# Performance work log

Hardware: AMD Instinct MI355X
Metric: run time of the kernel (lower is better)

## Reference

```python
import jax, jax.numpy as jnp
import numpy as np
from jax import lax

B, S, I = 256, 16, 64
D = 128
N_ITEMS = 100000
K = 3
PAD_ID = 0
BOS_ID = N_ITEMS
DILATIONS = (1, 2, 4)


def setup_inputs() -> dict:
    key = jax.random.key(0)
    ks = jax.random.split(key, 16)
    item_id = jax.random.randint(ks[0], (B, S, I), 0, N_ITEMS, dtype=jnp.int32)
    eval_from = jax.random.randint(ks[1], (B,), 0, S, dtype=jnp.int32)
    u_type = jax.random.randint(ks[2], (B,), 0, 4, dtype=jnp.int32)
    emb = jax.random.normal(ks[3], (N_ITEMS + 1, D), jnp.float32) * 0.05
    emb = emb.at[PAD_ID].set(0.0)  # padding_idx=0
    kaiming = (2.0 / (D * K)) ** 0.5
    conv_w0 = jax.random.normal(ks[4], (D, D, K), jnp.float32) * kaiming
    conv_w1 = jax.random.normal(ks[5], (D, D, K), jnp.float32) * kaiming
    conv_w2 = jax.random.normal(ks[6], (D, D, K), jnp.float32) * kaiming
    conv_b0 = jnp.zeros((D,), jnp.float32)
    conv_b1 = jnp.zeros((D,), jnp.float32)
    conv_b2 = jnp.zeros((D,), jnp.float32)
    gru_wih = jax.random.normal(ks[7], (3 * D, D), jnp.float32) * 0.05
    gru_whh = jax.random.normal(ks[8], (3 * D, D), jnp.float32) * 0.05
    gru_bih = jax.random.normal(ks[9], (3 * D,), jnp.float32) * 0.05
    gru_bhh = jax.random.normal(ks[10], (3 * D,), jnp.float32) * 0.05
    fus_w = jax.random.normal(ks[11], (D, 2 * D), jnp.float32) * 0.05
    fus_b = jnp.zeros((D,), jnp.float32)
    return {"item_id": item_id, "eval_from": eval_from, "u_type": u_type,
            "emb": emb,
            "conv_w0": conv_w0, "conv_b0": conv_b0,
            "conv_w1": conv_w1, "conv_b1": conv_b1,
            "conv_w2": conv_w2, "conv_b2": conv_b2,
            "gru_wih": gru_wih, "gru_whh": gru_whh,
            "gru_bih": gru_bih, "gru_bhh": gru_bhh,
            "fus_w": fus_w, "fus_b": fus_b}


def reference(item_id, eval_from, u_type, emb,
              conv_w0, conv_b0, conv_w1, conv_b1, conv_w2, conv_b2,
              gru_wih, gru_whh, gru_bih, gru_bhh, fus_w, fus_b):
    item_id = jnp.maximum(item_id, 0)  # clamp_min(0)
    Bc, Sc, Ic = item_id.shape
    convs = ((conv_w0, conv_b0, DILATIONS[0]),
             (conv_w1, conv_b1, DILATIONS[1]),
             (conv_w2, conv_b2, DILATIONS[2]))

    def tcn(x):  # x: [B, T, D] -> [B, T, D]
        h = jnp.transpose(x, (0, 2, 1))  # NCH
        for w, b, dil in convs:
            pad = (K - 1) * dil
            out = lax.conv_general_dilated(
                h, w, window_strides=(1,), padding=[(pad, 0)],
                rhs_dilation=(dil,),
                dimension_numbers=('NCH', 'OIH', 'NCH')) + b[None, :, None]
            h = jax.nn.relu(out + h)
        return jnp.transpose(h, (0, 2, 1))

    def gru_step(h, x):  # h,x: [B, D]
        gi = x @ gru_wih.T + gru_bih
        gh = h @ gru_whh.T + gru_bhh
        ir, iz, inn = jnp.split(gi, 3, axis=-1)
        hr, hz, hn = jnp.split(gh, 3, axis=-1)
        r = jax.nn.sigmoid(ir + hr)
        z = jax.nn.sigmoid(iz + hz)
        n = jnp.tanh(inn + r * hn)
        return (1.0 - z) * n + z * h

    pos = jnp.arange(Ic + 1)
    bos = jnp.full((Bc, 1), BOS_ID, dtype=item_id.dtype)

    def step(h, seq_s):  # seq_s: [B, I]
        lengths = (seq_s != PAD_ID).sum(-1)          # [B]
        max_len = lengths.max()                       # batch-level session max
        seq = jnp.concatenate([bos, seq_s], axis=1)   # [B, I+1], BOS prepended
        valid = pos[None, :] <= max_len               # positions torch keeps
        seq = jnp.where(valid, seq, PAD_ID)
        mask = seq != PAD_ID
        e = emb[seq]                                  # [B, I+1, D] (PAD row is 0)
        tc = tcn(e)
        fin = jnp.concatenate([tc, jnp.broadcast_to(h[:, None, :], tc.shape)], -1)
        reps = fin @ fus_w.T + fus_b                  # [B, I+1, D]
        reps = reps * valid[..., None]                # torch zero-pads beyond max_len
        # drop mask at last valid token (per-sample python loop in torch)
        mask = mask & ~((pos[None, :] == lengths[:, None]) & (lengths > 0)[:, None])
        mf = mask.astype(e.dtype)
        mean_emb = (e * mf[..., None]).sum(1) / jnp.maximum(mf.sum(1), 1.0)[:, None]
        h2 = gru_step(h, mean_emb)
        return h2, (reps, mask)

    h0 = jnp.zeros((Bc, D), jnp.float32)
    _, (reps, masks) = lax.scan(step, h0, jnp.transpose(item_id, (1, 0, 2)))
    reps = jnp.transpose(reps, (1, 0, 2, 3))          # [B, S, I+1, D]
    masks = jnp.transpose(masks, (1, 0, 2))           # [B, S, I+1]
    allow = jnp.arange(Sc)[None, :] >= eval_from[:, None]
    loss_masks = masks & allow[:, :, None]
    return reps, loss_masks, u_type
```

## Files before the change

kernel.cpp:

```cpp
#include <hip/hip_runtime.h>

#define BB 256
#define SS 16
#define II 64
#define DD 128
#define TT 65
#define BOS_ID 100000
#define XROW 256
#define XROWS 73
#define XT (XROWS*XROW)

#define OFF_LEN  0
#define OFF_ML   16384
#define OFF_ME   32768
#define OFF_HB   (32768 + 2097152)
#define OFF_WB2  (OFF_HB + 2097152)
#define OFF_WIHP (OFF_WB2 + 327680)
#define OFF_WGRU (OFF_WIHP + 98304)
#define OFF_GI   (OFF_WGRU + 131072)

#define OUT_MASK  (BB*SS*TT*DD)
#define OUT_UTYPE (OUT_MASK + BB*SS*TT)

typedef __attribute__((ext_vector_type(8))) short short8;
typedef __attribute__((ext_vector_type(4))) float f32x4;

__device__ __forceinline__ unsigned short f2bf(float f) {
    unsigned int u = __builtin_bit_cast(unsigned int, f);
    return (unsigned short)((u + 0x7fffu + ((u >> 16) & 1u)) >> 16);
}
__device__ __forceinline__ float bflo(unsigned int u) {
    return __builtin_bit_cast(float, u << 16);
}
__device__ __forceinline__ float bfhi(unsigned int u) {
    return __builtin_bit_cast(float, u & 0xffff0000u);
}
__device__ __forceinline__ void gld16(const void* g, void* l) {
    __builtin_amdgcn_global_load_lds(
        (const __attribute__((address_space(1))) void*)g,
        (__attribute__((address_space(3))) void*)l, 16, 0, 0);
}

__global__ __launch_bounds__(256) void prep_kernel(
    const float* __restrict__ w0, const float* __restrict__ w1,
    const float* __restrict__ w2, const float* __restrict__ fus_w,
    const float* __restrict__ wih, const float* __restrict__ whh,
    unsigned short* __restrict__ wB2,
    unsigned int* __restrict__ wih4, unsigned int* __restrict__ wgru4)
{
    int idx = blockIdx.x * 256 + threadIdx.x;
    if (idx < 163840) {
        int cid2  = idx >> 11;
        int inner = idx & 2047;
        int g = inner >> 9;
        int c = (inner >> 3) & 63;
        int e = inner & 7;
        int nh   = cid2 & 1;
        int rest = cid2 >> 1;
        int cq   = rest & 3;
        int m    = rest >> 2;
        int ci = cq * 32 + g * 8 + e;
        int co = nh * 64 + c;
        float v;
        if (m < 9) {
            int L = m / 3, k = m % 3;
            const float* w = (L == 0) ? w0 : ((L == 1) ? w1 : w2);
            v = w[(co * 128 + ci) * 3 + k];
            if (k == 2 && ci == co) v += 1.0f;
        } else {
            v = fus_w[co * 256 + ci];
        }
        wB2[idx] = f2bf(v);
    } else if (idx < 163840 + 24576) {
        int f   = idx - 163840;
        int dd4 = f / 1536;
        int rem = f - dd4 * 1536;
        int r   = rem >> 2;
        int c   = rem & 3;
        int d0  = 8 * dd4 + 2 * c;
        unsigned int lo = f2bf(wih[r * 128 + d0]);
        unsigned int hi = f2bf(wih[r * 128 + d0 + 1]);
        wih4[f] = (hi << 16) | lo;
    } else if (idx < 163840 + 24576 + 32768) {
        int f   = idx - 163840 - 24576;
        int dd4 = f >> 11;
        int rem = f & 2047;
        int r   = rem >> 2;
        int c   = rem & 3;
        int d0  = 8 * dd4 + 2 * c;
        float v0, v1;
        if (r < 384) { v0 = whh[r * 128 + d0]; v1 = whh[r * 128 + d0 + 1]; }
        else { const float* fw = fus_w + (r - 384) * 256 + 128;
               v0 = fw[d0]; v1 = fw[d0 + 1]; }
        wgru4[f] = ((unsigned int)f2bf(v1) << 16) | (unsigned int)f2bf(v0);
    }
}

__global__ __launch_bounds__(256) void len_kernel(
    const int* __restrict__ item_id, const int* __restrict__ u_type,
    int* __restrict__ lengths, int* __restrict__ maxlen,
    float* __restrict__ u_out)
{
    int s = blockIdx.x;
    int b = threadIdx.x;
    const int* row = item_id + (b * SS + s) * II;
    int cnt = 0;
    for (int i = 0; i < II; ++i) cnt += (row[i] > 0);
    lengths[b * SS + s] = cnt;
    __shared__ int red[256];
    red[b] = cnt;
    __syncthreads();
    for (int off = 128; off > 0; off >>= 1) {
        if (b < off) red[b] = max(red[b], red[b + off]);
        __syncthreads();
    }
    if (b == 0) maxlen[s] = red[0];
    if (s == 0) u_out[b] = (float)u_type[b];
}

__global__ __launch_bounds__(128) void mean_kernel(
    const int* __restrict__ item_id, const int* __restrict__ eval_from,
    const float* __restrict__ emb,
    const int* __restrict__ lengths, const int* __restrict__ maxlen,
    float* __restrict__ mean_emb, float* __restrict__ mask_out)
{
    int bid = blockIdx.x;
    int b = bid >> 4, s = bid & 15;
    int tid = threadIdx.x;
    __shared__ int seqs[TT];
    __shared__ int msk[TT];
    int ml  = maxlen[s];
    int len = lengths[bid];
    int ef  = eval_from[b];
    if (tid < TT) {
        int v;
        if (tid == 0) v = BOS_ID;
        else { int it = item_id[bid * II + tid - 1]; v = it > 0 ? it : 0; }
        if (tid > ml) v = 0;
        int m = (v != 0) && !(tid == len && len > 0);
        seqs[tid] = v;
        msk[tid]  = m;
        mask_out[bid * TT + tid] = (m && (s >= ef)) ? 1.0f : 0.0f;
    }
    __syncthreads();
    int cnt = 0;
    for (int p = 0; p < TT; ++p) cnt += msk[p];
    float acc = 0.0f;
    int d = tid;
    for (int p = 0; p < TT; ++p) {
        if (msk[p]) acc += emb[seqs[p] * DD + d];
    }
    mean_emb[bid * DD + d] = acc / (float)max(cnt, 1);
}

__global__ __launch_bounds__(384, 1) void gi_kernel(
    const float* __restrict__ me_all, const unsigned int* __restrict__ wih4,
    const float* __restrict__ bih, float* __restrict__ gi_all)
{
    __shared__ __align__(16) unsigned int wl[16 * 384 * 4];
    __shared__ __align__(16) float me[DD];
    int t   = threadIdx.x;
    int blk = blockIdx.x;
    {
        const unsigned char* g = (const unsigned char*)wih4 + t * 16;
        unsigned char* l = (unsigned char*)wl + t * 16;
#pragma unroll
        for (int i = 0; i < 16; ++i) gld16(g + i * 6144, l + i * 6144);
    }
    float bi = bih[t];
    asm volatile("s_waitcnt vmcnt(0)" ::: "memory");
    __syncthreads();
    const uint4* wl4 = (const uint4*)wl;
    for (int q = 0; q < 16; ++q) {
        int bs = blk * 16 + q;
        if (t < DD) me[t] = me_all[bs * DD + t];
        __syncthreads();
        float acc = bi;
#pragma unroll
        for (int dd4 = 0; dd4 < 16; ++dd4) {
            uint4 u = wl4[dd4 * 384 + t];
            float4 h0 = *(const float4*)&me[8 * dd4];
            float4 h1 = *(const float4*)&me[8 * dd4 + 4];
            acc += bflo(u.x) * h0.x + bfhi(u.x) * h0.y;
            acc += bflo(u.y) * h0.z + bfhi(u.y) * h0.w;
            acc += bflo(u.z) * h1.x + bfhi(u.z) * h1.y;
            acc += bflo(u.w) * h1.z + bfhi(u.w) * h1.w;
        }
        gi_all[bs * 384 + t] = acc;
        __syncthreads();
    }
}

__global__ __launch_bounds__(512, 1) void gru_kernel(
    const unsigned int* __restrict__ wgru4, const float* __restrict__ bhh,
    const float* __restrict__ fus_b, const float* __restrict__ gi_all,
    float* __restrict__ hB)
{
    __shared__ __align__(16) unsigned int hpk[64];
    __shared__ float g_z[DD], g_inn[DD], g_hn[DD];
    int t = threadIdx.x;
    int b = blockIdx.x;
    int j = t & 127;
    int grp = t >> 7;

    uint4 w[16];
    const uint4* wg4 = (const uint4*)wgru4;
#pragma unroll
    for (int dd4 = 0; dd4 < 16; ++dd4) w[dd4] = wg4[dd4 * 512 + t];

    float gi_r[SS];
#pragma unroll
    for (int s = 0; s < SS; ++s)
        gi_r[s] = (grp < 3) ? gi_all[(b * SS + s) * 384 + t] : 0.0f;

    float bias = (t < 384) ? bhh[t] : fus_b[j];
    float hj = 0.0f;
    if (t < 64) hpk[t] = 0u;
    __syncthreads();

    for (int s = 0; s < SS; ++s) {
        float acc = bias;
#pragma unroll
        for (int dd4 = 0; dd4 < 16; ++dd4) {
            uint4 hp = *(const uint4*)&hpk[dd4 * 4];
            uint4 u  = w[dd4];
            acc += bflo(u.x) * bflo(hp.x) + bfhi(u.x) * bfhi(hp.x);
            acc += bflo(u.y) * bflo(hp.y) + bfhi(u.y) * bfhi(hp.y);
            acc += bflo(u.z) * bflo(hp.z) + bfhi(u.z) * bfhi(hp.z);
            acc += bflo(u.w) * bflo(hp.w) + bfhi(u.w) * bfhi(hp.w);
        }
        if (grp == 3) {
            hB[(s * BB + b) * DD + j] = acc;
        } else if (grp == 1) { g_z[j] = gi_r[s] + acc; }
        else if (grp == 2)   { g_inn[j] = gi_r[s]; g_hn[j] = acc; }
        __syncthreads();
        if (grp == 0) {
            float r = 1.0f / (1.0f + expf(-(gi_r[s] + acc)));
            float z = 1.0f / (1.0f + expf(-g_z[j]));
            float n = tanhf(g_inn[j] + r * g_hn[j]);
            float hnew = (1.0f - z) * n + z * hj;
            hj = hnew;
            float hnb = __shfl_xor(hnew, 1);
            if ((j & 1) == 0) {
                unsigned int pk;
                asm("v_cvt_pk_bf16_f32 %0, %1, %2" : "=v"(pk) : "v"(hnew), "v"(hnb));
                hpk[j >> 1] = pk;
            }
        }
        __syncthreads();
    }
}

__global__ __launch_bounds__(256, 3) void tcn_kernel(
    const int* __restrict__ item_id, const float* __restrict__ emb,
    const int* __restrict__ maxlen,
    const unsigned short* __restrict__ wB2,
    const float* __restrict__ cb0, const float* __restrict__ cb1,
    const float* __restrict__ cb2,
    const float* __restrict__ hB, float* __restrict__ reps)
{
    __shared__ __align__(16) unsigned char lds_x[2][XT];
    __shared__ __align__(16) unsigned char ring[2][8192];

    const int tid = threadIdx.x, bid = blockIdx.x;
    const int lane = tid & 63, wv = tid >> 6;
    const int l15 = lane & 15, q4 = lane >> 4;
    const int t = wv >> 1, nh = wv & 1;
    const int tile = bid * 2 + t;
    const int b = tile >> 4, s = tile & 15;
    const int ml = maxlen[s];

    const unsigned char* wgbase = (const unsigned char*)wB2;
    unsigned char* xb = lds_x[t];

    {
        const unsigned char* src = wgbase + wv * 1024 + lane * 16;
        gld16(src,        &ring[0][wv * 1024]);
        gld16(src + 4096, &ring[0][4096 + wv * 1024]);
    }
    int* seqs2 = (int*)&ring[1][0];
    if (tid < 2 * TT) {
        int tt = tid / TT, p = tid - tt * TT;
        int tl = bid * 2 + tt;
        int v;
        if (p == 0) v = BOS_ID;
        else { int it = item_id[tl * II + p - 1]; v = it > 0 ? it : 0; }
        if (p > maxlen[tl & 15]) v = 0;
        seqs2[tt * TT + p] = v;
    }
    {
        float4 z = {0.f, 0.f, 0.f, 0.f};
        if (tid < 128) *(float4*)(lds_x[0] + tid * 16) = z;
        else           *(float4*)(lds_x[1] + (tid - 128) * 16) = z;
    }
    __syncthreads();

    for (int p = nh; p < TT; p += 2) {
        const float* er = emb + (long)seqs2[t * TT + p] * DD + lane * 2;
        float f0 = er[0], f1 = er[1];
        unsigned int pk = ((unsigned int)f2bf(f1) << 16) | (unsigned int)f2bf(f0);
        *(unsigned int*)(xb + (8 + p) * XROW + ((lane * 4) ^ ((p & 7) << 4))) = pk;
    }

    f32x4 acc[5][4];

#pragma unroll 1
    for (int cid = 0; cid < 40; ++cid) {
        int L = 0, cq, off, kq = 0;
        if (cid < 36) { L = cid / 12; kq = cid - L * 12; int k = kq >> 2; cq = kq & 3; off = (2 - k) << L; }
        else { cq = cid - 36; off = 0; }
        if (cid == 36 || (cid < 36 && kq == 0)) {
#pragma unroll
            for (int mt = 0; mt < 5; ++mt)
#pragma unroll
                for (int nt = 0; nt < 4; ++nt)
#pragma unroll
                    for (int r = 0; r < 4; ++r) acc[mt][nt][r] = 0.0f;
        }
        asm volatile("s_waitcnt vmcnt(0)" ::: "memory");
        __syncthreads();

        if (cid <= 38) {
            const unsigned char* src =
                wgbase + (size_t)(cid + 1) * 8192 + wv * 1024 + lane * 16;
            gld16(src,        &ring[(cid + 1) & 1][wv * 1024]);
            gld16(src + 4096, &ring[(cid + 1) & 1][4096 + wv * 1024]);
        }

        const unsigned char* sb = &ring[cid & 1][nh * 4096];
        const int xmask = ((l15 - off) & 7) << 4;
        const int colx  = (cq * 64 + q4 * 16) ^ xmask;
        short8 bfr[4], af[5];
#pragma unroll
        for (int nt = 0; nt < 4; ++nt)
            bfr[nt] = *(const short8*)(sb + q4 * 1024 + (nt * 16 + l15) * 16);
#pragma unroll
        for (int mt = 0; mt < 5; ++mt) {
            int rowA = 8 + mt * 16 + l15 - off;
            af[mt] = *(const short8*)(xb + rowA * XROW + colx);
        }
#pragma unroll
        for (int nt = 0; nt < 4; ++nt)
#pragma unroll
            for (int mt = 0; mt < 5; ++mt)
                acc[mt][nt] = __builtin_amdgcn_mfma_f32_16x16x32_bf16(
                    af[mt], bfr[nt], acc[mt][nt], 0, 0, 0);

        if (cid < 36 && kq == 11) {
            const float* cb = (L == 0) ? cb0 : ((L == 1) ? cb1 : cb2);
            __syncthreads();
#pragma unroll
            for (int nt = 0; nt < 4; ++nt) {
                float bia = cb[nh * 64 + nt * 16 + l15];
                int cbyte = nh * 128 + nt * 32 + l15 * 2;
#pragma unroll
                for (int mt = 0; mt < 5; ++mt)
#pragma unroll
                    for (int r = 0; r < 4; ++r) {
                        int p = mt * 16 + q4 * 4 + r;
                        if (p < TT) {
                            int row = 8 + p;
                            float v = acc[mt][nt][r] + bia;
                            *(unsigned short*)(xb + row * XROW +
                                               (cbyte ^ ((row & 7) << 4))) =
                                f2bf(v > 0.f ? v : 0.f);
                        }
                    }
            }
            __syncthreads();
        }
    }

    float hb[4];
#pragma unroll
    for (int nt = 0; nt < 4; ++nt)
        hb[nt] = hB[(s * BB + b) * DD + nh * 64 + nt * 16 + l15];
    long ob = (long)tile * (TT * DD);
#pragma unroll
    for (int mt = 0; mt < 5; ++mt)
#pragma unroll
        for (int nt = 0; nt < 4; ++nt)
#pragma unroll
            for (int r = 0; r < 4; ++r) {
                int p = mt * 16 + q4 * 4 + r;
                if (p < TT) {
                    float v = (p <= ml) ? (acc[mt][nt][r] + hb[nt]) : 0.0f;
                    reps[ob + p * DD + nh * 64 + nt * 16 + l15] = v;
                }
            }
}

extern "C" void kernel_launch(void* const* d_in, const int* in_sizes, int n_in,
                              void* d_out, int out_size, void* d_ws, size_t ws_size,
                              hipStream_t stream) {
    const int*   item_id   = (const int*)  d_in[0];
    const int*   eval_from = (const int*)  d_in[1];
    const int*   u_type    = (const int*)  d_in[2];
    const float* emb       = (const float*)d_in[3];
    const float* conv_w0   = (const float*)d_in[4];
    const float* conv_b0   = (const float*)d_in[5];
    const float* conv_w1   = (const float*)d_in[6];
    const float* conv_b1   = (const float*)d_in[7];
    const float* conv_w2   = (const float*)d_in[8];
    const float* conv_b2   = (const float*)d_in[9];
    const float* gru_wih   = (const float*)d_in[10];
    const float* gru_whh   = (const float*)d_in[11];
    const float* gru_bih   = (const float*)d_in[12];
    const float* gru_bhh   = (const float*)d_in[13];
    const float* fus_w     = (const float*)d_in[14];
    const float* fus_b     = (const float*)d_in[15];

    char* ws = (char*)d_ws;
    int*            lengths  = (int*)           (ws + OFF_LEN);
    int*            maxlen   = (int*)           (ws + OFF_ML);
    float*          mean_emb = (float*)         (ws + OFF_ME);
    float*          hB       = (float*)         (ws + OFF_HB);
    unsigned short* wB2      = (unsigned short*)(ws + OFF_WB2);
    unsigned int*   wih4     = (unsigned int*)  (ws + OFF_WIHP);
    unsigned int*   wgru4    = (unsigned int*)  (ws + OFF_WGRU);
    float*          gi_all   = (float*)         (ws + OFF_GI);

    float* out  = (float*)d_out;
    float* reps = out;
    float* mout = out + OUT_MASK;
    float* uout = out + OUT_UTYPE;

    prep_kernel<<<864, 256, 0, stream>>>(conv_w0, conv_w1, conv_w2, fus_w,
                                         gru_wih, gru_whh, wB2, wih4, wgru4);
    len_kernel<<<SS, 256, 0, stream>>>(item_id, u_type, lengths, maxlen, uout);
    mean_kernel<<<BB * SS, 128, 0, stream>>>(item_id, eval_from, emb, lengths, maxlen,
                                             mean_emb, mout);
    gi_kernel<<<BB, 384, 0, stream>>>(mean_emb, wih4, gru_bih, gi_all);
    gru_kernel<<<BB, 512, 0, stream>>>(wgru4, gru_bhh, fus_b, gi_all, hB);
    tcn_kernel<<<BB * SS / 2, 256, 0, stream>>>(item_id, emb, maxlen, wB2,
                                                conv_b0, conv_b1, conv_b2, hB, reps);
}
```

Measured before the change: 253.8 us.

## Load TCN weight fragments directly into registers with one-step prefetch

Drops the LDS double-buffered weight ring, which used global-to-LDS loads plus a waitcnt and a block-wide barrier every chunk. Each lane now reads its B-operand MFMA fragments straight from global memory into registers and prefetches the next chunk's fragments while the current one is computed. This removes the per-chunk barrier and frees 16 KB of LDS, but each wave fetches its own weight copy from global or L2 and the extra live registers may hurt occupancy.

```diff
diff --git a/kernel.cpp b/kernel.cpp
--- a/kernel.cpp
+++ b/kernel.cpp
@@ -260,7 +260,7 @@
     const float* __restrict__ hB, float* __restrict__ reps)
 {
     __shared__ __align__(16) unsigned char lds_x[2][XT];
-    __shared__ __align__(16) unsigned char ring[2][8192];
+    __shared__ int seqs2[2][TT];
 
     const int tid = threadIdx.x, bid = blockIdx.x;
     const int lane = tid & 63, wv = tid >> 6;
@@ -270,15 +270,10 @@
     const int b = tile >> 4, s = tile & 15;
     const int ml = maxlen[s];
 
-    const unsigned char* wgbase = (const unsigned char*)wB2;
     unsigned char* xb = lds_x[t];
-
-    {
-        const unsigned char* src = wgbase + wv * 1024 + lane * 16;
-        gld16(src,        &ring[0][wv * 1024]);
-        gld16(src + 4096, &ring[0][4096 + wv * 1024]);
-    }
-    int* seqs2 = (int*)&ring[1][0];
+    const unsigned char* wfrag =
+        (const unsigned char*)wB2 + nh * 4096 + q4 * 1024 + l15 * 16;
+
     if (tid < 2 * TT) {
         int tt = tid / TT, p = tid - tt * TT;
         int tl = bid * 2 + tt;
@@ -286,21 +281,26 @@
         if (p == 0) v = BOS_ID;
         else { int it = item_id[tl * II + p - 1]; v = it > 0 ? it : 0; }
         if (p > maxlen[tl & 15]) v = 0;
-        seqs2[tt * TT + p] = v;
+        seqs2[tt][p] = v;
     }
     {
         float4 z = {0.f, 0.f, 0.f, 0.f};
         if (tid < 128) *(float4*)(lds_x[0] + tid * 16) = z;
         else           *(float4*)(lds_x[1] + (tid - 128) * 16) = z;
     }
+    short8 wcur[4];
+#pragma unroll
+    for (int nt = 0; nt < 4; ++nt)
+        wcur[nt] = *(const short8*)(wfrag + nt * 256);
     __syncthreads();
 
     for (int p = nh; p < TT; p += 2) {
-        const float* er = emb + (long)seqs2[t * TT + p] * DD + lane * 2;
+        const float* er = emb + (long)seqs2[t][p] * DD + lane * 2;
         float f0 = er[0], f1 = er[1];
         unsigned int pk = ((unsigned int)f2bf(f1) << 16) | (unsigned int)f2bf(f0);
         *(unsigned int*)(xb + (8 + p) * XROW + ((lane * 4) ^ ((p & 7) << 4))) = pk;
     }
+    __syncthreads();
 
     f32x4 acc[5][4];
 
@@ -317,23 +317,18 @@
 #pragma unroll
                     for (int r = 0; r < 4; ++r) acc[mt][nt][r] = 0.0f;
         }
-        asm volatile("s_waitcnt vmcnt(0)" ::: "memory");
-        __syncthreads();
-
-        if (cid <= 38) {
-            const unsigned char* src =
-                wgbase + (size_t)(cid + 1) * 8192 + wv * 1024 + lane * 16;
-            gld16(src,        &ring[(cid + 1) & 1][wv * 1024]);
-            gld16(src + 4096, &ring[(cid + 1) & 1][4096 + wv * 1024]);
-        }
-
-        const unsigned char* sb = &ring[cid & 1][nh * 4096];
+
+        short8 wnxt[4];
+        if (cid < 39) {
+            const unsigned char* src = wfrag + (size_t)(cid + 1) * 8192;
+#pragma unroll
+            for (int nt = 0; nt < 4; ++nt)
+                wnxt[nt] = *(const short8*)(src + nt * 256);
+        }
+
         const int xmask = ((l15 - off) & 7) << 4;
         const int colx  = (cq * 64 + q4 * 16) ^ xmask;
-        short8 bfr[4], af[5];
-#pragma unroll
-        for (int nt = 0; nt < 4; ++nt)
-            bfr[nt] = *(const short8*)(sb + q4 * 1024 + (nt * 16 + l15) * 16);
+        short8 af[5];
 #pragma unroll
         for (int mt = 0; mt < 5; ++mt) {
             int rowA = 8 + mt * 16 + l15 - off;
@@ -344,7 +339,7 @@
 #pragma unroll
             for (int mt = 0; mt < 5; ++mt)
                 acc[mt][nt] = __builtin_amdgcn_mfma_f32_16x16x32_bf16(
-                    af[mt], bfr[nt], acc[mt][nt], 0, 0, 0);
+                    af[mt], wcur[nt], acc[mt][nt], 0, 0, 0);
 
         if (cid < 36 && kq == 11) {
             const float* cb = (L == 0) ? cb0 : ((L == 1) ? cb1 : cb2);
@@ -368,6 +363,11 @@
                     }
             }
             __syncthreads();
+        }
+
+        if (cid < 39) {
+#pragma unroll
+            for (int nt = 0; nt < 4; ++nt) wcur[nt] = wnxt[nt];
         }
     }
 
```

After: 293.4 us. 1.16x slower.

## Fuse len into prep kernel and gi projection into GRU kernel

Applied to the files above, without the earlier changes.

The length/maxlen computation becomes extra blocks of the weight-prep kernel, and the input-gate projection (W_ih · mean_emb) is computed inside the GRU recurrence kernel from LDS-resident bf16 weights. This removes two kernel launches and the gi_all round-trip through global memory. The trade-off is that the serial GRU loop now does the input projection each step, which lengthens the critical path per timestep, and the kernel carries 96KB of LDS.

```diff
diff --git a/kernel.cpp b/kernel.cpp
--- a/kernel.cpp
+++ b/kernel.cpp
@@ -17,7 +17,6 @@
 #define OFF_WB2  (OFF_HB + 2097152)
 #define OFF_WIHP (OFF_WB2 + 327680)
 #define OFF_WGRU (OFF_WIHP + 98304)
-#define OFF_GI   (OFF_WGRU + 131072)
 
 #define OUT_MASK  (BB*SS*TT*DD)
 #define OUT_UTYPE (OUT_MASK + BB*SS*TT)
@@ -45,9 +44,30 @@
     const float* __restrict__ w0, const float* __restrict__ w1,
     const float* __restrict__ w2, const float* __restrict__ fus_w,
     const float* __restrict__ wih, const float* __restrict__ whh,
+    const int* __restrict__ item_id, const int* __restrict__ u_type,
     unsigned short* __restrict__ wB2,
-    unsigned int* __restrict__ wih4, unsigned int* __restrict__ wgru4)
+    unsigned int* __restrict__ wih4, unsigned int* __restrict__ wgru4,
+    int* __restrict__ lengths, int* __restrict__ maxlen,
+    float* __restrict__ u_out)
 {
+    if (blockIdx.x >= 864) {
+        int s = blockIdx.x - 864;
+        int b = threadIdx.x;
+        const int* row = item_id + (b * SS + s) * II;
+        int cnt = 0;
+        for (int i = 0; i < II; ++i) cnt += (row[i] > 0);
+        lengths[b * SS + s] = cnt;
+        __shared__ int red[256];
+        red[b] = cnt;
+        __syncthreads();
+        for (int off = 128; off > 0; off >>= 1) {
+            if (b < off) red[b] = max(red[b], red[b + off]);
+            __syncthreads();
+        }
+        if (b == 0) maxlen[s] = red[0];
+        if (s == 0) u_out[b] = (float)u_type[b];
+        return;
+    }
     int idx = blockIdx.x * 256 + threadIdx.x;
     if (idx < 163840) {
         int cid2  = idx >> 11;
@@ -96,28 +116,6 @@
     }
 }
 
-__global__ __launch_bounds__(256) void len_kernel(
-    const int* __restrict__ item_id, const int* __restrict__ u_type,
-    int* __restrict__ lengths, int* __restrict__ maxlen,
-    float* __restrict__ u_out)
-{
-    int s = blockIdx.x;
-    int b = threadIdx.x;
-    const int* row = item_id + (b * SS + s) * II;
-    int cnt = 0;
-    for (int i = 0; i < II; ++i) cnt += (row[i] > 0);
-    lengths[b * SS + s] = cnt;
-    __shared__ int red[256];
-    red[b] = cnt;
-    __syncthreads();
-    for (int off = 128; off > 0; off >>= 1) {
-        if (b < off) red[b] = max(red[b], red[b + off]);
-        __syncthreads();
-    }
-    if (b == 0) maxlen[s] = red[0];
-    if (s == 0) u_out[b] = (float)u_type[b];
-}
-
 __global__ __launch_bounds__(128) void mean_kernel(
     const int* __restrict__ item_id, const int* __restrict__ eval_from,
     const float* __restrict__ emb,
@@ -153,73 +151,58 @@
     mean_emb[bid * DD + d] = acc / (float)max(cnt, 1);
 }
 
-__global__ __launch_bounds__(384, 1) void gi_kernel(
+__global__ __launch_bounds__(512, 1) void gru_kernel(
     const float* __restrict__ me_all, const unsigned int* __restrict__ wih4,
-    const float* __restrict__ bih, float* __restrict__ gi_all)
+    const float* __restrict__ bih,
+    const unsigned int* __restrict__ wgru4, const float* __restrict__ bhh,
+    const float* __restrict__ fus_b, float* __restrict__ hB)
 {
     __shared__ __align__(16) unsigned int wl[16 * 384 * 4];
-    __shared__ __align__(16) float me[DD];
-    int t   = threadIdx.x;
-    int blk = blockIdx.x;
-    {
-        const unsigned char* g = (const unsigned char*)wih4 + t * 16;
-        unsigned char* l = (unsigned char*)wl + t * 16;
-#pragma unroll
-        for (int i = 0; i < 16; ++i) gld16(g + i * 6144, l + i * 6144);
-    }
-    float bi = bih[t];
-    asm volatile("s_waitcnt vmcnt(0)" ::: "memory");
-    __syncthreads();
-    const uint4* wl4 = (const uint4*)wl;
-    for (int q = 0; q < 16; ++q) {
-        int bs = blk * 16 + q;
-        if (t < DD) me[t] = me_all[bs * DD + t];
-        __syncthreads();
-        float acc = bi;
-#pragma unroll
-        for (int dd4 = 0; dd4 < 16; ++dd4) {
-            uint4 u = wl4[dd4 * 384 + t];
-            float4 h0 = *(const float4*)&me[8 * dd4];
-            float4 h1 = *(const float4*)&me[8 * dd4 + 4];
-            acc += bflo(u.x) * h0.x + bfhi(u.x) * h0.y;
-            acc += bflo(u.y) * h0.z + bfhi(u.y) * h0.w;
-            acc += bflo(u.z) * h1.x + bfhi(u.z) * h1.y;
-            acc += bflo(u.w) * h1.z + bfhi(u.w) * h1.w;
-        }
-        gi_all[bs * 384 + t] = acc;
-        __syncthreads();
-    }
-}
-
-__global__ __launch_bounds__(512, 1) void gru_kernel(
-    const unsigned int* __restrict__ wgru4, const float* __restrict__ bhh,
-    const float* __restrict__ fus_b, const float* __restrict__ gi_all,
-    float* __restrict__ hB)
-{
-    __shared__ __align__(16) unsigned int hpk[64];
+    __shared__ __align__(16) float me[2][DD];
+    __shared__ unsigned int hpk[64];
     __shared__ float g_z[DD], g_inn[DD], g_hn[DD];
     int t = threadIdx.x;
     int b = blockIdx.x;
     int j = t & 127;
     int grp = t >> 7;
 
+    {
+        const unsigned char* g = (const unsigned char*)wih4 + t * 16;
+        unsigned char* l = (unsigned char*)wl + t * 16;
+#pragma unroll
+        for (int i = 0; i < 12; ++i) gld16(g + i * 8192, l + i * 8192);
+    }
     uint4 w[16];
     const uint4* wg4 = (const uint4*)wgru4;
 #pragma unroll
     for (int dd4 = 0; dd4 < 16; ++dd4) w[dd4] = wg4[dd4 * 512 + t];
 
-    float gi_r[SS];
-#pragma unroll
-    for (int s = 0; s < SS; ++s)
-        gi_r[s] = (grp < 3) ? gi_all[(b * SS + s) * 384 + t] : 0.0f;
-
-    float bias = (t < 384) ? bhh[t] : fus_b[j];
+    float bias_hh = (t < 384) ? bhh[t] : fus_b[j];
+    float bias_ih = (t < 384) ? bih[t] : 0.0f;
+    if (t < DD) me[0][t] = me_all[b * SS * DD + t];
     float hj = 0.0f;
     if (t < 64) hpk[t] = 0u;
+    asm volatile("s_waitcnt vmcnt(0)" ::: "memory");
     __syncthreads();
 
+    const uint4* wl4 = (const uint4*)wl;
     for (int s = 0; s < SS; ++s) {
-        float acc = bias;
+        if (t < DD && s < 15) me[(s + 1) & 1][t] = me_all[(b * SS + s + 1) * DD + t];
+        const float* mc = me[s & 1];
+        float gi = bias_ih;
+        if (grp < 3) {
+#pragma unroll
+            for (int dd4 = 0; dd4 < 16; ++dd4) {
+                uint4 u = wl4[dd4 * 384 + t];
+                float4 m0 = *(const float4*)&mc[8 * dd4];
+                float4 m1 = *(const float4*)&mc[8 * dd4 + 4];
+                gi += bflo(u.x) * m0.x + bfhi(u.x) * m0.y;
+                gi += bflo(u.y) * m0.z + bfhi(u.y) * m0.w;
+                gi += bflo(u.z) * m1.x + bfhi(u.z) * m1.y;
+                gi += bflo(u.w) * m1.z + bfhi(u.w) * m1.w;
+            }
+        }
+        float acc = bias_hh;
 #pragma unroll
         for (int dd4 = 0; dd4 < 16; ++dd4) {
             uint4 hp = *(const uint4*)&hpk[dd4 * 4];
@@ -231,11 +214,11 @@
         }
         if (grp == 3) {
             hB[(s * BB + b) * DD + j] = acc;
-        } else if (grp == 1) { g_z[j] = gi_r[s] + acc; }
-        else if (grp == 2)   { g_inn[j] = gi_r[s]; g_hn[j] = acc; }
+        } else if (grp == 1) { g_z[j] = gi + acc; }
+        else if (grp == 2)   { g_inn[j] = gi; g_hn[j] = acc; }
         __syncthreads();
         if (grp == 0) {
-            float r = 1.0f / (1.0f + expf(-(gi_r[s] + acc)));
+            float r = 1.0f / (1.0f + expf(-(gi + acc)));
             float z = 1.0f / (1.0f + expf(-g_z[j]));
             float n = tanhf(g_inn[j] + r * g_hn[j]);
             float hnew = (1.0f - z) * n + z * hj;
@@ -418,20 +401,19 @@
     unsigned short* wB2      = (unsigned short*)(ws + OFF_WB2);
     unsigned int*   wih4     = (unsigned int*)  (ws + OFF_WIHP);
     unsigned int*   wgru4    = (unsigned int*)  (ws + OFF_WGRU);
-    float*          gi_all   = (float*)         (ws + OFF_GI);
 
     float* out  = (float*)d_out;
     float* reps = out;
     float* mout = out + OUT_MASK;
     float* uout = out + OUT_UTYPE;
 
-    prep_kernel<<<864, 256, 0, stream>>>(conv_w0, conv_w1, conv_w2, fus_w,
-                                         gru_wih, gru_whh, wB2, wih4, wgru4);
-    len_kernel<<<SS, 256, 0, stream>>>(item_id, u_type, lengths, maxlen, uout);
+    prep_kernel<<<880, 256, 0, stream>>>(conv_w0, conv_w1, conv_w2, fus_w,
+                                         gru_wih, gru_whh, item_id, u_type,
+                                         wB2, wih4, wgru4, lengths, maxlen, uout);
     mean_kernel<<<BB * SS, 128, 0, stream>>>(item_id, eval_from, emb, lengths, maxlen,
                                              mean_emb, mout);
-    gi_kernel<<<BB, 384, 0, stream>>>(mean_emb, wih4, gru_bih, gi_all);
-    gru_kernel<<<BB, 512, 0, stream>>>(wgru4, gru_bhh, fus_b, gi_all, hB);
+    gru_kernel<<<BB, 512, 0, stream>>>(mean_emb, wih4, gru_bih,
+                                       wgru4, gru_bhh, fus_b, hB);
     tcn_kernel<<<BB * SS / 2, 256, 0, stream>>>(item_id, emb, maxlen, wB2,
                                                 conv_b0, conv_b1, conv_b2, hB, reps);
 }
```

Result: faster. 243.2 us (-4.2%).
